# Performance work log

Measured on AMD Instinct MI355X. Metric: run time of the kernel, lower is better.

The kernel has to match this reference:

```python
import jax, jax.numpy as jnp
import numpy as np

B, S, P = 64, 1024, 1024
D_IN, D, OUT = 50, 300, 1024
LN_EPS = 1e-6  # custom LayerNorm in repo-style code (a_2/b_2, eps=1e-6)


def setup_inputs() -> dict:
    key = jax.random.key(0)
    ks = jax.random.split(key, 16)
    std = 1e-4  # matches torch .normal_(mean=0, std=0.0001)
    return {
        "x": jax.random.normal(ks[0], (B, S, D_IN), jnp.float32),
        "matrix_embed": jax.random.normal(ks[1], (D_IN, D), jnp.float32),
        "past": jax.random.normal(ks[2], (B, P, D_IN), jnp.float32),
        "w_pt": jax.random.normal(ks[3], (D_IN, D), jnp.float32) * std,
        "b_pt": jax.random.normal(ks[4], (1, D), jnp.float32) * std,
        "w_pg": jax.random.normal(ks[5], (D_IN, D), jnp.float32) * std,
        "b_pg": jax.random.normal(ks[6], (1, D), jnp.float32) * std,
        "w_ps": jax.random.normal(ks[7], (D_IN, D), jnp.float32) * std,
        "b_ps": jax.random.normal(ks[8], (1, D), jnp.float32) * std,
        "w_ex": jax.random.normal(ks[9], (D_IN, D), jnp.float32) * std,
        "b_ex": jax.random.normal(ks[10], (1, D), jnp.float32) * std,
        "ln_g": jnp.ones((D,), jnp.float32),
        "ln_b": jnp.zeros((D,), jnp.float32),
        "W1": jax.random.normal(ks[11], (D, D), jnp.float32) * 0.05,
        "b1": jnp.zeros((D,), jnp.float32),
        "W2": jax.random.normal(ks[12], (D, OUT), jnp.float32) * 0.05,
        "b2": jnp.zeros((OUT,), jnp.float32),
    }


def _layernorm(h, g, b):
    mu = jnp.mean(h, axis=-1, keepdims=True)
    var = jnp.mean(jnp.square(h - mu), axis=-1, keepdims=True)
    return g * (h - mu) / jnp.sqrt(var + LN_EPS) + b


def reference(x, matrix_embed, past, w_pt, b_pt, w_pg, b_pg, w_ps, b_ps,
              w_ex, b_ex, ln_g, ln_b, W1, b1, W2, b2):
    # token: [B,S,300]
    token = _layernorm(x @ matrix_embed, ln_g, ln_b)
    past_token = jnp.tanh(x @ w_pt + b_pt)          # [B,S,300]
    past_vector = jnp.tanh(past @ w_pg + b_pg)      # [B,P,300]
    past_gate = jax.nn.sigmoid(jnp.einsum('bsd,bpd->bsp', past_token, past_vector))
    past_state = jnp.tanh(past @ w_ps + b_ps)       # [B,P,300]
    pre_state = past_gate @ past_state              # [B,S,300]
    expose_vector = jnp.tanh(x @ w_ex + b_ex)       # [B,S,300]
    expose_gate = jax.nn.sigmoid(jnp.einsum('bsd,btd->bst', expose_vector, pre_state))
    filter_token = token + expose_gate @ pre_state  # [B,S,300]
    # output MLP (dropout is identity in eval mode)
    h = jax.nn.relu(filter_token @ W1 + b1)
    return h @ W2 + b2
```

## Files before the change

kernel.cpp:

```cpp
#include <hip/hip_runtime.h>
#include <hip/hip_bf16.h>
#include <math.h>

typedef __attribute__((ext_vector_type(8))) short bf16x8;
typedef __attribute__((ext_vector_type(4))) float f32x4;

__device__ inline float bf2f(short u) {
  union { float f; unsigned int i; } v;
  v.i = ((unsigned int)(unsigned short)u) << 16;
  return v.f;
}
__device__ inline short f2bf(float f) {
  union { float f; unsigned int i; } v; v.f = f;
  unsigned int r = v.i + 0x7fff + ((v.i >> 16) & 1);
  return (short)(r >> 16);
}

__global__ void pad_rows(const float* __restrict__ src, short* __restrict__ dst,
                         int C, int Cp, int total) {
  int i = blockIdx.x * 256 + threadIdx.x;
  if (i >= total) return;
  int r = i / Cp, c = i - r * Cp;
  dst[i] = f2bf(c < C ? src[(size_t)r * C + c] : 0.f);
}

__global__ void pad_T(const float* __restrict__ src, short* __restrict__ dst,
                      int K, int N, int Kp, int total) {
  int i = blockIdx.x * 256 + threadIdx.x;
  if (i >= total) return;
  int n = i / Kp, k = i - n * Kp;
  dst[i] = f2bf((k < K && n < N) ? src[(size_t)k * N + n] : 0.f);
}

__global__ __launch_bounds__(256) void transpose_pd(const short* __restrict__ in,
                                                    short* __restrict__ out) {
  __shared__ unsigned int T[64][32];
  const int b = blockIdx.z, p0 = blockIdx.x * 64, d0 = blockIdx.y * 64;
  const short* ib = in + (size_t)b * 1024 * 320;
  short* ob = out + (size_t)b * 320 * 1024;
  for (int i = threadIdx.x; i < 512; i += 256) {
    int p = i >> 3, g = i & 7;
    uint4 v = *(const uint4*)&ib[(size_t)(p0 + p) * 320 + d0 + g * 8];
    int s = p & 31;
    T[p][(4 * g + 0) ^ s] = v.x;
    T[p][(4 * g + 1) ^ s] = v.y;
    T[p][(4 * g + 2) ^ s] = v.z;
    T[p][(4 * g + 3) ^ s] = v.w;
  }
  __syncthreads();
  for (int i = threadIdx.x; i < 512; i += 256) {
    int d = i >> 3, g = i & 7;
    int w0 = d >> 1;
    __align__(16) unsigned short tmp[8];
#pragma unroll
    for (int j = 0; j < 8; ++j) {
      int p = g * 8 + j;
      unsigned int val = T[p][w0 ^ (p & 31)];
      tmp[j] = (d & 1) ? (unsigned short)(val >> 16) : (unsigned short)(val & 0xffff);
    }
    *(uint4*)&ob[(size_t)(d0 + d) * 1024 + p0 + g * 8] = *(const uint4*)tmp;
  }
}

template<int NT, int MODE>
__global__ __launch_bounds__(512) void gemm_ep(
    const short* __restrict__ A, const short* __restrict__ Bt, int K,
    const float* __restrict__ bias, int biasN,
    void* __restrict__ outp, int outStride)
{
  __shared__ __align__(16) short Bst[NT][40];
  const int tid = threadIdx.x;
  const int wave = tid >> 6, lane = tid & 63;
  const int m = lane & 15, quad = lane >> 4;
  const int row0 = blockIdx.x * 128 + wave * 16;
  const int n0 = blockIdx.y * NT;

  f32x4 zero = {0.f, 0.f, 0.f, 0.f};
  f32x4 acc[NT / 16];
#pragma unroll
  for (int i = 0; i < NT / 16; ++i) acc[i] = zero;

  const short* arow = A + (size_t)(row0 + m) * K;

  for (int k0 = 0; k0 < K; k0 += 32) {
    __syncthreads();
    for (int idx = tid; idx < NT * 4; idx += 512) {
      int n = idx >> 2, kc = (idx & 3) << 3;
      *(uint4*)&Bst[n][kc] = *(const uint4*)&Bt[(size_t)(n0 + n) * K + k0 + kc];
    }
    __syncthreads();
    bf16x8 af = *(const bf16x8*)(arow + k0 + quad * 8);
#pragma unroll
    for (int nt = 0; nt < NT / 16; ++nt) {
      bf16x8 bf = *(const bf16x8*)&Bst[nt * 16 + m][quad * 8];
      acc[nt] = __builtin_amdgcn_mfma_f32_16x16x32_bf16(af, bf, acc[nt], 0, 0, 0);
    }
  }

#pragma unroll
  for (int nt = 0; nt < NT / 16; ++nt) {
#pragma unroll
    for (int r = 0; r < 4; ++r) {
      int row = row0 + quad * 4 + r;
      int col = n0 + nt * 16 + m;
      float v = acc[nt][r];
      if (MODE != 0) v += (col < biasN) ? bias[col] : 0.f;
      if (MODE == 1) v = tanhf(v);
      if (MODE == 2) v = fmaxf(v, 0.f);
      if (MODE == 3)
        ((float*)outp)[(size_t)row * outStride + col] = v;
      else
        ((short*)outp)[(size_t)row * outStride + col] = f2bf(v);
    }
  }
}

__global__ __launch_bounds__(256) void ln_rows(short* __restrict__ tp,
                                               const float* __restrict__ g,
                                               const float* __restrict__ bb) {
  const int wave = threadIdx.x >> 6, lane = threadIdx.x & 63;
  const int row = blockIdx.x * 4 + wave;
  short* p = tp + (size_t)row * 320;
  float vals[5], s = 0.f, ss = 0.f;
#pragma unroll
  for (int i = 0; i < 5; ++i) {
    int c = lane + i * 64;
    float v = (c < 300) ? bf2f(p[c]) : 0.f;
    vals[i] = v; s += v; ss += v * v;
  }
#pragma unroll
  for (int off = 32; off > 0; off >>= 1) { s += __shfl_down(s, off); ss += __shfl_down(ss, off); }
  s = __shfl(s, 0); ss = __shfl(ss, 0);
  const float mu = s * (1.f / 300.f);
  const float rstd = rsqrtf(ss * (1.f / 300.f) - mu * mu + 1e-6f);
#pragma unroll
  for (int i = 0; i < 5; ++i) {
    int c = lane + i * 64;
    float v = (c < 300) ? (g[c] * (vals[i] - mu) * rstd + bb[c]) : 0.f;
    p[c] = f2bf(v);
  }
}

__device__ inline void gload16(const short* g, short* l) {
  __builtin_amdgcn_global_load_lds((const __attribute__((address_space(1))) void*)g,
                                   (__attribute__((address_space(3))) void*)l, 16, 0, 0);
}
__device__ inline void block_sync() {
  asm volatile("s_waitcnt vmcnt(0) lgkmcnt(0)" ::: "memory");
  __builtin_amdgcn_s_barrier();
  __builtin_amdgcn_sched_barrier(0);
}

__global__ __launch_bounds__(256, 2) void attn_v4(
    const short* __restrict__ Qm, const short* __restrict__ Km,
    const short* __restrict__ VT, const short* __restrict__ tokp,
    short* __restrict__ Outp)
{
  __shared__ __align__(16) short KsL[2][10240];
  __shared__ __align__(16) short PsL[2][2560];

  const int tid = threadIdx.x;
  const int wave = tid >> 6, lane = tid & 63;
  const int m = lane & 15, quad = lane >> 4;
  const int b = blockIdx.x;
  const int qrow0 = b * 1024 + blockIdx.y * 64;
  const size_t kbase = (size_t)b * 1024 * 320;
  const short* vtb = VT + (size_t)b * 320 * 1024;

  if (wave < 2) {
    bf16x8 qf[2][10];
    const short* qb = Qm + (size_t)(qrow0 + wave * 32 + m) * 320;
#pragma unroll
    for (int h = 0; h < 2; ++h)
#pragma unroll
      for (int c = 0; c < 10; ++c)
        qf[h][c] = *(const bf16x8*)(qb + h * 5120 + c * 32 + quad * 8);
    const int par = m & 1;

    block_sync();

    for (int pt = 0; pt < 32; ++pt) {
      const short* Kc = &KsL[pt & 1][0];
      f32x4 s00 = {0.f, 0.f, 0.f, 0.f}, s01 = s00, s10 = s00, s11 = s00;
      __builtin_amdgcn_s_setprio(1);
#pragma unroll
      for (int c = 0; c < 10; ++c) {
        int cc = c ^ par;
        bf16x8 b0 = *(const bf16x8*)&Kc[m * 320 + cc * 32 + quad * 8];
        bf16x8 b1 = *(const bf16x8*)&Kc[(m + 16) * 320 + cc * 32 + quad * 8];
        s00 = __builtin_amdgcn_mfma_f32_16x16x32_bf16(qf[0][c], b0, s00, 0, 0, 0);
        s10 = __builtin_amdgcn_mfma_f32_16x16x32_bf16(qf[1][c], b0, s10, 0, 0, 0);
        s01 = __builtin_amdgcn_mfma_f32_16x16x32_bf16(qf[0][c], b1, s01, 0, 0, 0);
        s11 = __builtin_amdgcn_mfma_f32_16x16x32_bf16(qf[1][c], b1, s11, 0, 0, 0);
      }
      __builtin_amdgcn_s_setprio(0);
      short* Pb = &PsL[pt & 1][0];
#pragma unroll
      for (int h = 0; h < 2; ++h) {
        const int qt = wave * 2 + h;
#pragma unroll
        for (int g = 0; g < 2; ++g) {
          f32x4 sv = h ? (g ? s11 : s10) : (g ? s01 : s00);
#pragma unroll
          for (int r = 0; r < 4; ++r) {
            float v = 1.f / (1.f + __expf(-sv[r]));
            Pb[(qt * 16 + quad * 4 + r) * 40 + g * 16 + m] = f2bf(v);
          }
        }
      }
      block_sync();
    }
  } else {
    const int v = wave - 2;
    const short* spk[10];
#pragma unroll
    for (int s = 0; s < 10; ++s) {
      int c = (v * 10 + s) * 64 + lane;
      int p = c / 40, ch = c - p * 40;
      spk[s] = Km + kbase + (size_t)p * 320 + (ch ^ ((p & 1) << 2)) * 8;
    }
    const short* vtB = vtb + (size_t)(v * 160 + m) * 1024 + quad * 8;

    f32x4 zero = {0.f, 0.f, 0.f, 0.f};
    f32x4 o[4][10];
#pragma unroll
    for (int i = 0; i < 4; ++i)
#pragma unroll
      for (int j = 0; j < 10; ++j) o[i][j] = zero;

    auto stageK = [&](int pt) {
#pragma unroll
      for (int s = 0; s < 10; ++s)
        gload16(spk[s] + (size_t)pt * 10240, &KsL[pt & 1][(v * 10 + s) * 64 * 8]);
    };

    auto pv_step = [&](int t) {
      const short* Pr = &PsL[t & 1][0];
      bf16x8 pa[4];
#pragma unroll
      for (int qt = 0; qt < 4; ++qt)
        pa[qt] = *(const bf16x8*)&Pr[(qt * 16 + m) * 40 + quad * 8];
      const short* vp = vtB + t * 32;
      __builtin_amdgcn_s_setprio(1);
#pragma unroll
      for (int dt = 0; dt < 10; ++dt) {
        bf16x8 vb = *(const bf16x8*)(vp + dt * 16384);
#pragma unroll
        for (int qt = 0; qt < 4; ++qt)
          o[qt][dt] = __builtin_amdgcn_mfma_f32_16x16x32_bf16(pa[qt], vb, o[qt][dt], 0, 0, 0);
      }
      __builtin_amdgcn_s_setprio(0);
    };

    stageK(0);
    block_sync();

    for (int pt = 0; pt < 32; ++pt) {
      if (pt < 31) stageK(pt + 1);
      if (pt > 0) pv_step(pt - 1);
      block_sync();
    }
    pv_step(31);

#pragma unroll
    for (int qt = 0; qt < 4; ++qt)
#pragma unroll
      for (int dt = 0; dt < 10; ++dt)
#pragma unroll
        for (int r = 0; r < 4; ++r) {
          const size_t row = (size_t)qrow0 + qt * 16 + quad * 4 + r;
          const int col = v * 160 + dt * 16 + m;
          float val = o[qt][dt][r];
          if (tokp) val += bf2f(tokp[row * 320 + col]);
          Outp[row * 320 + col] = f2bf(val);
        }
  }
}

extern "C" void kernel_launch(void* const* d_in, const int* in_sizes, int n_in,
                              void* d_out, int out_size, void* d_ws, size_t ws_size,
                              hipStream_t stream)
{
  const float* x    = (const float*)d_in[0];
  const float* me   = (const float*)d_in[1];
  const float* past = (const float*)d_in[2];
  const float* wpt  = (const float*)d_in[3];
  const float* bpt  = (const float*)d_in[4];
  const float* wpg  = (const float*)d_in[5];
  const float* bpg  = (const float*)d_in[6];
  const float* wps  = (const float*)d_in[7];
  const float* bps  = (const float*)d_in[8];
  const float* wex  = (const float*)d_in[9];
  const float* bex  = (const float*)d_in[10];
  const float* lng  = (const float*)d_in[11];
  const float* lnb  = (const float*)d_in[12];
  const float* W1   = (const float*)d_in[13];
  const float* b1   = (const float*)d_in[14];
  const float* W2   = (const float*)d_in[15];
  const float* b2   = (const float*)d_in[16];
  float* out = (float*)d_out;

  char* ws = (char*)d_ws;
  size_t off = 0;
  auto alloc = [&](size_t bytes) -> char* {
    char* p = ws + off; off += (bytes + 255) & ~(size_t)255; return p;
  };
  const size_t RB = 65536ull;
  short* xp    = (short*)alloc(RB * 64 * 2);
  short* pastp = (short*)alloc(RB * 64 * 2);
  short* wmeT  = (short*)alloc(320 * 64 * 2);
  short* wptT  = (short*)alloc(320 * 64 * 2);
  short* wpgT  = (short*)alloc(320 * 64 * 2);
  short* wpsT  = (short*)alloc(320 * 64 * 2);
  short* wexT  = (short*)alloc(320 * 64 * 2);
  short* w1T   = (short*)alloc(320 * 320 * 2);
  short* w2T   = (short*)alloc(1024ull * 320 * 2);
  short* buf0  = (short*)alloc(RB * 320 * 2);
  short* buf1  = (short*)alloc(RB * 320 * 2);
  short* buf2  = (short*)alloc(RB * 320 * 2);
  short* buf3  = (short*)alloc(RB * 320 * 2);
  short* vtbuf = (short*)alloc(RB * 320 * 2);

  {
    int total = 65536 * 64;
    pad_rows<<<dim3((total + 255) / 256), 256, 0, stream>>>(x, xp, 50, 64, total);
    pad_rows<<<dim3((total + 255) / 256), 256, 0, stream>>>(past, pastp, 50, 64, total);
  }
  {
    int t = 320 * 64;
    dim3 g((t + 255) / 256);
    pad_T<<<g, 256, 0, stream>>>(me,  wmeT, 50, 300, 64, t);
    pad_T<<<g, 256, 0, stream>>>(wpt, wptT, 50, 300, 64, t);
    pad_T<<<g, 256, 0, stream>>>(wpg, wpgT, 50, 300, 64, t);
    pad_T<<<g, 256, 0, stream>>>(wps, wpsT, 50, 300, 64, t);
    pad_T<<<g, 256, 0, stream>>>(wex, wexT, 50, 300, 64, t);
  }
  { int t = 320 * 320;  pad_T<<<(t + 255) / 256, 256, 0, stream>>>(W1, w1T, 300, 300, 320, t); }
  { int t = 1024 * 320; pad_T<<<(t + 255) / 256, 256, 0, stream>>>(W2, w2T, 300, 1024, 320, t); }

  dim3 g512(512, 1);
  dim3 tgrid(16, 5, 64);
  gemm_ep<320, 1><<<g512, 512, 0, stream>>>(xp,    wptT, 64, bpt, 300, buf0, 320);
  gemm_ep<320, 1><<<g512, 512, 0, stream>>>(pastp, wpgT, 64, bpg, 300, buf1, 320);
  gemm_ep<320, 1><<<g512, 512, 0, stream>>>(pastp, wpsT, 64, bps, 300, buf2, 320);
  transpose_pd<<<tgrid, 256, 0, stream>>>(buf2, vtbuf);

  attn_v4<<<dim3(64, 16), 256, 0, stream>>>(buf0, buf1, vtbuf, nullptr, buf3);

  gemm_ep<320, 0><<<g512, 512, 0, stream>>>(xp, wmeT, 64, nullptr, 0, buf1, 320);
  ln_rows<<<16384, 256, 0, stream>>>(buf1, lng, lnb);
  gemm_ep<320, 1><<<g512, 512, 0, stream>>>(xp, wexT, 64, bex, 300, buf2, 320);

  transpose_pd<<<tgrid, 256, 0, stream>>>(buf3, vtbuf);

  attn_v4<<<dim3(64, 16), 256, 0, stream>>>(buf2, buf3, vtbuf, buf1, buf0);

  gemm_ep<320, 2><<<g512, 512, 0, stream>>>(buf0, w1T, 320, b1, 300, buf3, 320);
  gemm_ep<256, 3><<<dim3(512, 4), 512, 0, stream>>>(buf3, w2T, 320, b2, 1024, out, 1024);
}
```

Before: 1.052 ms.

## Move K staging to QK waves, widen LDS swizzle, prefetch V before P reads

The K-tile global-to-LDS staging moves from the PV waves to the QK/sigmoid waves, which now prefetch the next tile themselves. The K swizzle changes from a 1-bit parity XOR to an XOR over row&7 to cut LDS bank conflicts, and the P buffer row stride shrinks from 40 to 36. In the PV step, all ten V fragments are now loaded from global memory before the P fragments are read from LDS, so load latency overlaps the MFMA work. The cost is extra issue load and VGPRs on the QK waves and higher register pressure on the PV waves.

Result: slower. 1.100 ms (+4.6%).

```diff
diff --git a/kernel.cpp b/kernel.cpp
--- a/kernel.cpp
+++ b/kernel.cpp
@@ -151,13 +151,13 @@
   __builtin_amdgcn_sched_barrier(0);
 }
 
-__global__ __launch_bounds__(256, 2) void attn_v4(
+__global__ __launch_bounds__(256, 2) void attn_v5(
     const short* __restrict__ Qm, const short* __restrict__ Km,
     const short* __restrict__ VT, const short* __restrict__ tokp,
     short* __restrict__ Outp)
 {
   __shared__ __align__(16) short KsL[2][10240];
-  __shared__ __align__(16) short PsL[2][2560];
+  __shared__ __align__(16) short PsL[2][2304];
 
   const int tid = threadIdx.x;
   const int wave = tid >> 6, lane = tid & 63;
@@ -168,6 +168,15 @@
   const short* vtb = VT + (size_t)b * 320 * 1024;
 
   if (wave < 2) {
+    unsigned off_k[10];
+#pragma unroll
+    for (int j = 0; j < 10; ++j) {
+      int c = wave * 64 + j * 128 + lane;
+      int p = c / 40, ch = c - p * 40;
+      off_k[j] = (unsigned)(p * 640 + ((ch ^ (p & 7)) << 4));
+    }
+    const char* kg = (const char*)(Km + kbase);
+
     bf16x8 qf[2][10];
     const short* qb = Qm + (size_t)(qrow0 + wave * 32 + m) * 320;
 #pragma unroll
@@ -175,19 +184,27 @@
 #pragma unroll
       for (int c = 0; c < 10; ++c)
         qf[h][c] = *(const bf16x8*)(qb + h * 5120 + c * 32 + quad * 8);
-    const int par = m & 1;
-
+
+#pragma unroll
+    for (int j = 0; j < 10; ++j)
+      gload16((const short*)(kg + off_k[j]), &KsL[0][(wave * 64 + j * 128) * 8]);
     block_sync();
 
     for (int pt = 0; pt < 32; ++pt) {
+      if (pt < 31) {
+#pragma unroll
+        for (int j = 0; j < 10; ++j)
+          gload16((const short*)(kg + (size_t)(pt + 1) * 20480 + off_k[j]),
+                  &KsL[(pt + 1) & 1][(wave * 64 + j * 128) * 8]);
+      }
       const short* Kc = &KsL[pt & 1][0];
       f32x4 s00 = {0.f, 0.f, 0.f, 0.f}, s01 = s00, s10 = s00, s11 = s00;
       __builtin_amdgcn_s_setprio(1);
 #pragma unroll
       for (int c = 0; c < 10; ++c) {
-        int cc = c ^ par;
-        bf16x8 b0 = *(const bf16x8*)&Kc[m * 320 + cc * 32 + quad * 8];
-        bf16x8 b1 = *(const bf16x8*)&Kc[(m + 16) * 320 + cc * 32 + quad * 8];
+        int ch0 = ((4 * c + quad) ^ (m & 7)) * 8;
+        bf16x8 b0 = *(const bf16x8*)&Kc[m * 320 + ch0];
+        bf16x8 b1 = *(const bf16x8*)&Kc[(m + 16) * 320 + ch0];
         s00 = __builtin_amdgcn_mfma_f32_16x16x32_bf16(qf[0][c], b0, s00, 0, 0, 0);
         s10 = __builtin_amdgcn_mfma_f32_16x16x32_bf16(qf[1][c], b0, s10, 0, 0, 0);
         s01 = __builtin_amdgcn_mfma_f32_16x16x32_bf16(qf[0][c], b1, s01, 0, 0, 0);
@@ -204,22 +221,15 @@
 #pragma unroll
           for (int r = 0; r < 4; ++r) {
             float v = 1.f / (1.f + __expf(-sv[r]));
-            Pb[(qt * 16 + quad * 4 + r) * 40 + g * 16 + m] = f2bf(v);
+            Pb[(qt * 16 + quad * 4 + r) * 36 + g * 16 + m] = f2bf(v);
           }
         }
       }
       block_sync();
     }
   } else {
-    const int v = wave - 2;
-    const short* spk[10];
-#pragma unroll
-    for (int s = 0; s < 10; ++s) {
-      int c = (v * 10 + s) * 64 + lane;
-      int p = c / 40, ch = c - p * 40;
-      spk[s] = Km + kbase + (size_t)p * 320 + (ch ^ ((p & 1) << 2)) * 8;
-    }
-    const short* vtB = vtb + (size_t)(v * 160 + m) * 1024 + quad * 8;
+    const int dsl = wave - 2;
+    const short* vtB = vtb + (size_t)(dsl * 160 + m) * 1024 + quad * 8;
 
     f32x4 zero = {0.f, 0.f, 0.f, 0.f};
     f32x4 o[4][10];
@@ -228,35 +238,35 @@
 #pragma unroll
       for (int j = 0; j < 10; ++j) o[i][j] = zero;
 
-    auto stageK = [&](int pt) {
-#pragma unroll
-      for (int s = 0; s < 10; ++s)
-        gload16(spk[s] + (size_t)pt * 10240, &KsL[pt & 1][(v * 10 + s) * 64 * 8]);
-    };
-
     auto pv_step = [&](int t) {
       const short* Pr = &PsL[t & 1][0];
+      const short* vp = vtB + t * 32;
+      bf16x8 va[5], vb5[5];
+#pragma unroll
+      for (int u = 0; u < 5; ++u) va[u] = *(const bf16x8*)(vp + u * 16384);
+#pragma unroll
+      for (int u = 0; u < 5; ++u) vb5[u] = *(const bf16x8*)(vp + (u + 5) * 16384);
       bf16x8 pa[4];
 #pragma unroll
       for (int qt = 0; qt < 4; ++qt)
-        pa[qt] = *(const bf16x8*)&Pr[(qt * 16 + m) * 40 + quad * 8];
-      const short* vp = vtB + t * 32;
+        pa[qt] = *(const bf16x8*)&Pr[(qt * 16 + m) * 36 + quad * 8];
       __builtin_amdgcn_s_setprio(1);
 #pragma unroll
-      for (int dt = 0; dt < 10; ++dt) {
-        bf16x8 vb = *(const bf16x8*)(vp + dt * 16384);
+      for (int dt = 0; dt < 5; ++dt)
 #pragma unroll
         for (int qt = 0; qt < 4; ++qt)
-          o[qt][dt] = __builtin_amdgcn_mfma_f32_16x16x32_bf16(pa[qt], vb, o[qt][dt], 0, 0, 0);
-      }
+          o[qt][dt] = __builtin_amdgcn_mfma_f32_16x16x32_bf16(pa[qt], va[dt], o[qt][dt], 0, 0, 0);
+#pragma unroll
+      for (int dt = 5; dt < 10; ++dt)
+#pragma unroll
+        for (int qt = 0; qt < 4; ++qt)
+          o[qt][dt] = __builtin_amdgcn_mfma_f32_16x16x32_bf16(pa[qt], vb5[dt - 5], o[qt][dt], 0, 0, 0);
       __builtin_amdgcn_s_setprio(0);
     };
 
-    stageK(0);
     block_sync();
 
     for (int pt = 0; pt < 32; ++pt) {
-      if (pt < 31) stageK(pt + 1);
       if (pt > 0) pv_step(pt - 1);
       block_sync();
     }
@@ -269,7 +279,7 @@
 #pragma unroll
         for (int r = 0; r < 4; ++r) {
           const size_t row = (size_t)qrow0 + qt * 16 + quad * 4 + r;
-          const int col = v * 160 + dt * 16 + m;
+          const int col = dsl * 160 + dt * 16 + m;
           float val = o[qt][dt][r];
           if (tokp) val += bf2f(tokp[row * 320 + col]);
           Outp[row * 320 + col] = f2bf(val);
@@ -345,7 +355,7 @@
   gemm_ep<320, 1><<<g512, 512, 0, stream>>>(pastp, wpsT, 64, bps, 300, buf2, 320);
   transpose_pd<<<tgrid, 256, 0, stream>>>(buf2, vtbuf);
 
-  attn_v4<<<dim3(64, 16), 256, 0, stream>>>(buf0, buf1, vtbuf, nullptr, buf3);
+  attn_v5<<<dim3(64, 16), 256, 0, stream>>>(buf0, buf1, vtbuf, nullptr, buf3);
 
   gemm_ep<320, 0><<<g512, 512, 0, stream>>>(xp, wmeT, 64, nullptr, 0, buf1, 320);
   ln_rows<<<16384, 256, 0, stream>>>(buf1, lng, lnb);
@@ -353,7 +363,7 @@
 
   transpose_pd<<<tgrid, 256, 0, stream>>>(buf3, vtbuf);
 
-  attn_v4<<<dim3(64, 16), 256, 0, stream>>>(buf2, buf3, vtbuf, buf1, buf0);
+  attn_v5<<<dim3(64, 16), 256, 0, stream>>>(buf2, buf3, vtbuf, buf1, buf0);
 
   gemm_ep<320, 2><<<g512, 512, 0, stream>>>(buf0, w1T, 320, b1, 300, buf3, 320);
   gemm_ep<256, 3><<<dim3(512, 4), 512, 0, stream>>>(buf3, w2T, 320, b2, 1024, out, 1024);
```
